# Performance work log

Hardware: AMD Instinct MI355X
Metric: run time of the kernel (lower is better)

Reference implementation:

```python
import jax, jax.numpy as jnp
import numpy as np

TEMPERATURE = 0.5
EPS = 1e-12  # torch F.normalize eps


def setup_inputs() -> dict:
    key = jax.random.key(0)
    k1, k2 = jax.random.split(key)
    z_i = jax.random.normal(k1, (32, 128, 128), dtype=jnp.float32)
    z_j = jax.random.normal(k2, (32, 128, 128), dtype=jnp.float32)
    return {"z_i": z_i, "z_j": z_j}


def _l2_normalize(x):
    # matches torch F.normalize(dim=1): x / max(||x||, eps)
    n = jnp.sqrt(jnp.sum(x * x, axis=1, keepdims=True))
    return x / jnp.maximum(n, EPS)


def _off_diagonal(a):
    # rows of a with the diagonal removed, row-major order -> [n, n-1]
    n = a.shape[0]
    return a.reshape(-1)[:-1].reshape(n - 1, n + 1)[:, 1:].reshape(n, n - 1)


def reference(z_i, z_j):
    B, S, D = z_i.shape
    N = B * S
    zi = _l2_normalize(z_i.reshape(N, D))
    zj = _l2_normalize(z_j.reshape(N, D))
    r = jnp.concatenate([zi, zj], axis=0)              # [2N, D]
    sim = r @ r.T                                      # [2N, 2N]
    # positives: off-diagonals at +/-N (unaffected by the diag -inf fill)
    pos = jnp.concatenate([jnp.diagonal(sim, N), jnp.diagonal(sim, -N)])  # [2N]
    # negatives: all non-diagonal entries, row-major (== torch boolean-mask view)
    neg = _off_diagonal(sim)                           # [2N, 2N-1]
    logits = jnp.concatenate([pos[:, None], neg], axis=1) / TEMPERATURE  # [2N, 2N]
    # labels are all 0 -> CE(sum) / 2N == mean of -log_softmax[:, 0]
    loss = -jax.nn.log_softmax(logits, axis=1)[:, 0]
    return jnp.sum(loss) / (2 * N)
```

## Files before the change

### kernel.cpp

```cpp
#include <hip/hip_runtime.h>
#include <hip/hip_bf16.h>
#include <math.h>

#define NPAIR 4096
#define D 128
#define TWO_N 8192
#define NJC 8
#define NPART (NJC * 2)

typedef short bf16x8 __attribute__((ext_vector_type(8)));
typedef float f32x4 __attribute__((ext_vector_type(4)));

__device__ inline unsigned short f2bf(float x) {
    union { float f; unsigned u; } v; v.f = x;
    unsigned u = v.u;
    unsigned r = u + 0x7fffu + ((u >> 16) & 1u);
    return (unsigned short)(r >> 16);
}

__global__ __launch_bounds__(256) void norm_kernel(const float* __restrict__ zi,
                                                   const float* __restrict__ zj,
                                                   unsigned int* __restrict__ Rb,
                                                   float* __restrict__ pos) {
    int k = blockIdx.x * 4 + (threadIdx.x >> 6);
    int t = threadIdx.x & 63;
    const float2 a = *(const float2*)(zi + k * D + 2 * t);
    const float2 b = *(const float2*)(zj + k * D + 2 * t);
    float si = a.x * a.x + a.y * a.y;
    float sj = b.x * b.x + b.y * b.y;
    float dt = a.x * b.x + a.y * b.y;
    #pragma unroll
    for (int m = 1; m < 64; m <<= 1) {
        si += __shfl_xor(si, m, 64);
        sj += __shfl_xor(sj, m, 64);
        dt += __shfl_xor(dt, m, 64);
    }
    float ii = 1.0f / fmaxf(sqrtf(si), 1e-12f);
    float ij = 1.0f / fmaxf(sqrtf(sj), 1e-12f);
    unsigned short b0 = f2bf(a.x * ii), b1 = f2bf(a.y * ii);
    Rb[k * (D / 2) + t] = (unsigned)b0 | ((unsigned)b1 << 16);
    b0 = f2bf(b.x * ij); b1 = f2bf(b.y * ij);
    Rb[(k + NPAIR) * (D / 2) + t] = (unsigned)b0 | ((unsigned)b1 << 16);
    if (t == 0) pos[k] = dt * ii * ij;
}

__global__ __launch_bounds__(256, 2) void simexp_kernel(const uint4* __restrict__ Rb,
                                                        float* __restrict__ rspart) {
    __shared__ uint4 As[16 * 128];
    __shared__ uint4 Bs[16 * 128];
    const int bi = blockIdx.x >> 3, jc = blockIdx.x & 7;
    const int tid = threadIdx.x;

    #pragma unroll
    for (int it = 0; it < 8; ++it) {
        int slot = it * 256 + tid;
        int row = (slot & 15) + ((slot >> 8) << 4);
        int c = (slot >> 4) & 15;
        As[c * 128 + row] = Rb[(bi * 128 + row) * 16 + c];
    }

    const int wave = tid >> 6, lane = tid & 63;
    const int rp = lane & 15, q = lane >> 4;
    const int wr = (wave & 1) * 64;
    const int wc = (wave >> 1) * 64;

    float rs[16];
    #pragma unroll
    for (int i = 0; i < 16; ++i) rs[i] = 0.f;

    for (int jt = 0; jt < 8; ++jt) {
        const int colbase = jc * 1024 + jt * 128;
        __syncthreads();
        #pragma unroll
        for (int it = 0; it < 8; ++it) {
            int slot = it * 256 + tid;
            int row = (slot & 15) + ((slot >> 8) << 4);
            int c = (slot >> 4) & 15;
            Bs[c * 128 + row] = Rb[(colbase + row) * 16 + c];
        }
        __syncthreads();

        f32x4 acc[4][4] = {};
        #pragma unroll
        for (int kt = 0; kt < 4; ++kt) {
            bf16x8 afr[4], bfr[4];
            const int cb = (kt * 4 + q) * 128;
            #pragma unroll
            for (int rt = 0; rt < 4; ++rt)
                afr[rt] = *(const bf16x8*)&As[cb + wr + rt * 16 + rp];
            #pragma unroll
            for (int ct = 0; ct < 4; ++ct)
                bfr[ct] = *(const bf16x8*)&Bs[cb + wc + ct * 16 + rp];
            #pragma unroll
            for (int rt = 0; rt < 4; ++rt)
                #pragma unroll
                for (int ct = 0; ct < 4; ++ct)
                    acc[rt][ct] = __builtin_amdgcn_mfma_f32_16x16x32_bf16(
                        afr[rt], bfr[ct], acc[rt][ct], 0, 0, 0);
        }

        if (colbase == bi * 128) {
            #pragma unroll
            for (int rt = 0; rt < 4; ++rt)
                #pragma unroll
                for (int r = 0; r < 4; ++r) {
                    int ro = wr + q * 4 + rt * 16 + r;
                    float s = 0.f;
                    #pragma unroll
                    for (int ct = 0; ct < 4; ++ct) {
                        int co = wc + ct * 16 + rp;
                        float x = acc[rt][ct][r];
                        float e = __expf(x + x);
                        s += (ro == co) ? 0.f : e;
                    }
                    rs[rt * 4 + r] += s;
                }
        } else {
            #pragma unroll
            for (int rt = 0; rt < 4; ++rt)
                #pragma unroll
                for (int r = 0; r < 4; ++r) {
                    float s = 0.f;
                    #pragma unroll
                    for (int ct = 0; ct < 4; ++ct) {
                        float x = acc[rt][ct][r];
                        s += __expf(x + x);
                    }
                    rs[rt * 4 + r] += s;
                }
        }
    }

    #pragma unroll
    for (int i = 0; i < 16; ++i) {
        float v = rs[i];
        v += __shfl_xor(v, 1, 64);
        v += __shfl_xor(v, 2, 64);
        v += __shfl_xor(v, 4, 64);
        v += __shfl_xor(v, 8, 64);
        rs[i] = v;
    }
    if (rp == 0) {
        const int slab = jc * 2 + (wave >> 1);
        const int rowb = bi * 128 + wr + q * 4;
        #pragma unroll
        for (int rt = 0; rt < 4; ++rt)
            #pragma unroll
            for (int r = 0; r < 4; ++r)
                rspart[slab * TWO_N + rowb + rt * 16 + r] = rs[rt * 4 + r];
    }
}

__global__ __launch_bounds__(1024) void finalize_kernel(const float* __restrict__ rspart,
                                                        const float* __restrict__ pos,
                                                        float* __restrict__ out) {
    __shared__ float red[16];
    int tid = threadIdx.x;
    float local = 0.f;
    #pragma unroll
    for (int i = 0; i < TWO_N / 1024; ++i) {
        int k = i * 1024 + tid;
        float rsum = 0.f;
        #pragma unroll
        for (int p = 0; p < NPART; ++p) rsum += rspart[p * TWO_N + k];
        float ps = pos[k & (NPAIR - 1)];
        float p2 = ps + ps;
        float denom = rsum + __expf(p2);
        local += logf(denom) - p2;
    }
    #pragma unroll
    for (int m = 1; m < 64; m <<= 1) local += __shfl_xor(local, m, 64);
    if ((tid & 63) == 0) red[tid >> 6] = local;
    __syncthreads();
    if (tid == 0) {
        float s = 0.f;
        #pragma unroll
        for (int w = 0; w < 16; ++w) s += red[w];
        out[0] = s / (float)TWO_N;
    }
}

extern "C" void kernel_launch(void* const* d_in, const int* in_sizes, int n_in,
                              void* d_out, int out_size, void* d_ws, size_t ws_size,
                              hipStream_t stream) {
    const float* zi = (const float*)d_in[0];
    const float* zj = (const float*)d_in[1];
    char* ws = (char*)d_ws;
    unsigned int* Rb = (unsigned int*)ws;
    float* rspart = (float*)(ws + 2 * 1024 * 1024);
    float* pos = (float*)(ws + 2 * 1024 * 1024 + 512 * 1024);

    norm_kernel<<<NPAIR / 4, 256, 0, stream>>>(zi, zj, Rb, pos);
    simexp_kernel<<<64 * NJC, 256, 0, stream>>>((const uint4*)Rb, rspart);
    finalize_kernel<<<1, 1024, 0, stream>>>(rspart, pos, (float*)d_out);
}
```

Before: 92.38 us.

## Double-buffer B tiles with async global-to-LDS loads, keep A in registers

The sim/exp kernel now loads the A fragments straight from global into registers once, which removes the A shared-memory tile. B tiles are double-buffered in LDS using global_load_lds async copies with an XOR-swizzled layout, so the next tile's load overlaps the current MFMA work and one barrier per iteration goes away. The finalize step is spread over 16 blocks that combine results by atomicAdd into an output zeroed in norm_kernel. This risks a race if the async loads are not waited on before use, and the atomics make the float summation order nondeterministic.

```diff
diff --git a/kernel.cpp b/kernel.cpp
--- a/kernel.cpp
+++ b/kernel.cpp
@@ -11,6 +11,12 @@
 typedef short bf16x8 __attribute__((ext_vector_type(8)));
 typedef float f32x4 __attribute__((ext_vector_type(4)));
 
+__device__ __forceinline__ void async_ld16(void* lds, const void* g) {
+    __builtin_amdgcn_global_load_lds(
+        (__attribute__((address_space(1))) const unsigned int*)g,
+        (__attribute__((address_space(3))) unsigned int*)lds, 16, 0, 0);
+}
+
 __device__ inline unsigned short f2bf(float x) {
     union { float f; unsigned u; } v; v.f = x;
     unsigned u = v.u;
@@ -21,7 +27,9 @@
 __global__ __launch_bounds__(256) void norm_kernel(const float* __restrict__ zi,
                                                    const float* __restrict__ zj,
                                                    unsigned int* __restrict__ Rb,
-                                                   float* __restrict__ pos) {
+                                                   float* __restrict__ pos,
+                                                   float* __restrict__ out) {
+    if (blockIdx.x == 0 && threadIdx.x == 0) out[0] = 0.f;
     int k = blockIdx.x * 4 + (threadIdx.x >> 6);
     int t = threadIdx.x & 63;
     const float2 a = *(const float2*)(zi + k * D + 2 * t);
@@ -46,60 +54,71 @@
 
 __global__ __launch_bounds__(256, 2) void simexp_kernel(const uint4* __restrict__ Rb,
                                                         float* __restrict__ rspart) {
-    __shared__ uint4 As[16 * 128];
-    __shared__ uint4 Bs[16 * 128];
+    __shared__ uint4 Bs[2][2048];
     const int bi = blockIdx.x >> 3, jc = blockIdx.x & 7;
     const int tid = threadIdx.x;
-
-    #pragma unroll
-    for (int it = 0; it < 8; ++it) {
-        int slot = it * 256 + tid;
-        int row = (slot & 15) + ((slot >> 8) << 4);
-        int c = (slot >> 4) & 15;
-        As[c * 128 + row] = Rb[(bi * 128 + row) * 16 + c];
-    }
-
     const int wave = tid >> 6, lane = tid & 63;
     const int rp = lane & 15, q = lane >> 4;
     const int wr = (wave & 1) * 64;
     const int wc = (wave >> 1) * 64;
 
+    bf16x8 afr[4][4];
+    {
+        const uint4* Ab = Rb + (bi * 128 + wr + rp) * 16;
+        #pragma unroll
+        for (int kt = 0; kt < 4; ++kt)
+            #pragma unroll
+            for (int rt = 0; rt < 4; ++rt)
+                afr[kt][rt] = *(const bf16x8*)&Ab[rt * 256 + kt * 4 + q];
+    }
+
+    const int rl15 = wave * 4 + q;
+    const int laneoff = rl15 * 256 + ((rp ^ rl15) << 4);
+    const char* Rbb = (const char*)Rb;
+
     float rs[16];
     #pragma unroll
     for (int i = 0; i < 16; ++i) rs[i] = 0.f;
 
+    {
+        const char* g = Rbb + (jc * 1024) * 256 + laneoff;
+        char* l = (char*)&Bs[0][0] + wave * 1024;
+        #pragma unroll
+        for (int it = 0; it < 8; ++it)
+            async_ld16(l + it * 4096, g + it * 4096);
+    }
+
     for (int jt = 0; jt < 8; ++jt) {
-        const int colbase = jc * 1024 + jt * 128;
         __syncthreads();
-        #pragma unroll
-        for (int it = 0; it < 8; ++it) {
-            int slot = it * 256 + tid;
-            int row = (slot & 15) + ((slot >> 8) << 4);
-            int c = (slot >> 4) & 15;
-            Bs[c * 128 + row] = Rb[(colbase + row) * 16 + c];
+
+        if (jt < 7) {
+            const char* g = Rbb + (jc * 1024 + (jt + 1) * 128) * 256 + laneoff;
+            char* l = (char*)&Bs[(jt + 1) & 1][0] + wave * 1024;
+            #pragma unroll
+            for (int it = 0; it < 8; ++it)
+                async_ld16(l + it * 4096, g + it * 4096);
         }
-        __syncthreads();
-
+
+        const uint4* B = &Bs[jt & 1][0];
         f32x4 acc[4][4] = {};
         #pragma unroll
         for (int kt = 0; kt < 4; ++kt) {
-            bf16x8 afr[4], bfr[4];
-            const int cb = (kt * 4 + q) * 128;
-            #pragma unroll
-            for (int rt = 0; rt < 4; ++rt)
-                afr[rt] = *(const bf16x8*)&As[cb + wr + rt * 16 + rp];
-            #pragma unroll
-            for (int ct = 0; ct < 4; ++ct)
-                bfr[ct] = *(const bf16x8*)&Bs[cb + wc + ct * 16 + rp];
+            const int k = kt * 4 + q;
+            bf16x8 bfr[4];
+            #pragma unroll
+            for (int ct = 0; ct < 4; ++ct) {
+                const int crow = wc + ct * 16 + rp;
+                bfr[ct] = *(const bf16x8*)&B[crow * 16 + (k ^ rp)];
+            }
             #pragma unroll
             for (int rt = 0; rt < 4; ++rt)
                 #pragma unroll
                 for (int ct = 0; ct < 4; ++ct)
                     acc[rt][ct] = __builtin_amdgcn_mfma_f32_16x16x32_bf16(
-                        afr[rt], bfr[ct], acc[rt][ct], 0, 0, 0);
+                        afr[kt][rt], bfr[ct], acc[rt][ct], 0, 0, 0);
         }
 
-        if (colbase == bi * 128) {
+        if (jc * 1024 + jt * 128 == bi * 128) {
             #pragma unroll
             for (int rt = 0; rt < 4; ++rt)
                 #pragma unroll
@@ -151,32 +170,29 @@
     }
 }
 
-__global__ __launch_bounds__(1024) void finalize_kernel(const float* __restrict__ rspart,
-                                                        const float* __restrict__ pos,
-                                                        float* __restrict__ out) {
-    __shared__ float red[16];
+__global__ __launch_bounds__(256) void finalize_kernel(const float* __restrict__ rspart,
+                                                       const float* __restrict__ pos,
+                                                       float* __restrict__ out) {
+    __shared__ float red[4];
     int tid = threadIdx.x;
     float local = 0.f;
     #pragma unroll
-    for (int i = 0; i < TWO_N / 1024; ++i) {
-        int k = i * 1024 + tid;
+    for (int i = 0; i < 2; ++i) {
+        int k = blockIdx.x * 512 + i * 256 + tid;
         float rsum = 0.f;
         #pragma unroll
         for (int p = 0; p < NPART; ++p) rsum += rspart[p * TWO_N + k];
         float ps = pos[k & (NPAIR - 1)];
         float p2 = ps + ps;
-        float denom = rsum + __expf(p2);
-        local += logf(denom) - p2;
+        local += logf(rsum + __expf(p2)) - p2;
     }
     #pragma unroll
     for (int m = 1; m < 64; m <<= 1) local += __shfl_xor(local, m, 64);
     if ((tid & 63) == 0) red[tid >> 6] = local;
     __syncthreads();
     if (tid == 0) {
-        float s = 0.f;
-        #pragma unroll
-        for (int w = 0; w < 16; ++w) s += red[w];
-        out[0] = s / (float)TWO_N;
+        float s = red[0] + red[1] + red[2] + red[3];
+        atomicAdd(out, s * (1.0f / (float)TWO_N));
     }
 }
 
@@ -190,7 +206,7 @@
     float* rspart = (float*)(ws + 2 * 1024 * 1024);
     float* pos = (float*)(ws + 2 * 1024 * 1024 + 512 * 1024);
 
-    norm_kernel<<<NPAIR / 4, 256, 0, stream>>>(zi, zj, Rb, pos);
+    norm_kernel<<<NPAIR / 4, 256, 0, stream>>>(zi, zj, Rb, pos, (float*)d_out);
     simexp_kernel<<<64 * NJC, 256, 0, stream>>>((const uint4*)Rb, rspart);
-    finalize_kernel<<<1, 1024, 0, stream>>>(rspart, pos, (float*)d_out);
-}
+    finalize_kernel<<<16, 256, 0, stream>>>(rspart, pos, (float*)d_out);
+}
```

New measurement: 86.26 us. 1.07x faster.
